# Performance work log

Measured on AMD Instinct MI355X. Metric: run time of the kernel, lower is better.

Reference implementation:

```python
import jax, jax.numpy as jnp
import numpy as np

NUM_NODE = 100000
DEG = 16
E = NUM_NODE * DEG
IN_C = 128
HID_C = 128
NUM_REL = 8


def setup_inputs() -> dict:
    key = jax.random.key(0)
    k1, k2, k3, k4, k5, k6 = jax.random.split(key, 6)
    x = jax.random.normal(k1, (NUM_NODE, IN_C), dtype=jnp.float32)
    # glorot-style init for relation weights [num_rel, in, hid]
    scale = jnp.sqrt(6.0 / (IN_C + HID_C)).astype(jnp.float32)
    rel_weight = jax.random.uniform(k2, (NUM_REL, IN_C, HID_C), dtype=jnp.float32, minval=-1.0, maxval=1.0) * scale
    # uniform-degree CSR so every node has deg >= 1 (avoids div-by-zero, matches module assumption)
    ptr = jnp.arange(NUM_NODE + 1, dtype=jnp.int64) * DEG
    idx = jax.random.randint(k3, (E,), 0, NUM_NODE, dtype=jnp.int64)
    edge_types = jax.random.randint(k4, (E,), 0, NUM_REL, dtype=jnp.int64)
    # about 1/3 of nodes have cached history (value != -1)
    history_map = jax.random.randint(k5, (NUM_NODE,), -1, 2, dtype=jnp.int64)
    history_buffer = jax.random.normal(k6, (NUM_NODE, HID_C), dtype=jnp.float32)
    return {
        'x': x,
        'rel_weight': rel_weight,
        'ptr': ptr,
        'idx': idx,
        'edge_types': edge_types,
        'history_map': history_map,
        'history_buffer': history_buffer,
        'history_size': 1,
        'num_node': NUM_NODE,
    }


def reference(x, rel_weight, ptr, idx, edge_types, history_map, history_buffer, history_size, num_node):
    E_ = idx.shape[0]
    num_rel = rel_weight.shape[0]
    hid = rel_weight.shape[2]
    xg = x[idx]                                   # [E, in] gather of source features
    # relation-grouped transform: small static loop over relations, masked accumulate
    msgs = jnp.zeros((E_, hid), dtype=x.dtype)
    for r in range(num_rel):
        msgs = msgs + jnp.where((edge_types == r)[:, None], xg @ rel_weight[r], jnp.zeros((), x.dtype))
    deg = ptr[1:] - ptr[:-1]                      # [num_node]
    seg = jnp.repeat(jnp.arange(num_node), deg, total_repeat_length=E_)  # dst id per edge
    out = jax.ops.segment_sum(msgs, seg, num_segments=num_node)          # scatter-sum
    out = out / deg[:, None].astype(out.dtype)    # degree normalization
    if history_size > 0:                          # static python int
        out = jnp.where((history_map != -1)[:, None], history_buffer, out)
    return (out, out)
```

## Files before the change

### kernel.cpp

```cpp
#include <hip/hip_runtime.h>
#include <stdint.h>

#define IN_C   128
#define HID_C  128
#define NREL   8
#define K_TOTAL (NREL * IN_C)
#define KHALF   512
#define TILE_M  16
#define SROW    520

typedef float  f32x4  __attribute__((ext_vector_type(4)));
typedef __bf16 bf16x8 __attribute__((ext_vector_type(8)));
typedef short  s16x8  __attribute__((ext_vector_type(8)));

__device__ __forceinline__ unsigned short f2bf(float f) {
    unsigned int u = __float_as_uint(f);
    u += 0x7fffu + ((u >> 16) & 1u);
    return (unsigned short)(u >> 16);
}

__global__ void zero_count_kernel(unsigned int* count) { *count = 0u; }

__global__ __launch_bounds__(256) void prep_kernel(
        const float* __restrict__ W, const int* __restrict__ hmap,
        unsigned short* __restrict__ Wt, int* __restrict__ list,
        unsigned int* __restrict__ count, int NN, int WE) {
    int tid = blockIdx.x * blockDim.x + threadIdx.x;
    if (tid < NN) {
        if (hmap[tid] == -1) {
            unsigned int p = atomicAdd(count, 1u);
            list[p] = tid;
        }
    }
    if (tid < WE) {
        int r   = tid >> 14;
        int rem = tid & 16383;
        int k   = rem >> 7;
        int c   = rem & 127;
        Wt[(size_t)c * K_TOTAL + r * IN_C + k] = f2bf(W[tid]);
    }
}

__global__ __launch_bounds__(256) void history_kernel(
        const int* __restrict__ hmap, const float* __restrict__ hbuf,
        float* __restrict__ out, int NN) {
    int gid = blockIdx.x * blockDim.x + threadIdx.x;
    int n = gid >> 5;
    int q = gid & 31;
    if (n >= NN) return;
    if (hmap[n] != -1) {
        const f32x4* src = (const f32x4*)hbuf;
        f32x4 v = src[(size_t)n * 32 + q];
        f32x4* o = (f32x4*)out;
        o[(size_t)n * 32 + q] = v;
        o[(size_t)NN * 32 + (size_t)n * 32 + q] = v;
    }
}

__global__ __launch_bounds__(256) void gemm_kernel(
        const float* __restrict__ x,
        const int* __restrict__ ptr,
        const int* __restrict__ idx,
        const int* __restrict__ ety,
        const unsigned short* __restrict__ Wt,
        const int* __restrict__ list,
        const unsigned int* __restrict__ count,
        float* __restrict__ out, int NN) {
    __shared__ float S[TILE_M * SROW];
    __shared__ int   nids[TILE_M];
    __shared__ float invdeg[TILE_M];

    unsigned int cnt = *count;
    int rowbase = blockIdx.x * TILE_M;
    if (rowbase >= (int)cnt) return;

    int t = threadIdx.x;
    if (t < TILE_M) {
        int row = rowbase + t;
        int nid = -1; float idg = 0.f;
        if (row < (int)cnt) {
            nid = list[row];
            int d = ptr[nid + 1] - ptr[nid];
            idg = 1.0f / (float)d;
        }
        nids[t] = nid;
        invdeg[t] = idg;
    }

    f32x4 acc0 = {0.f, 0.f, 0.f, 0.f};
    f32x4 acc1 = {0.f, 0.f, 0.f, 0.f};
    int wave   = t >> 6;
    int lane   = t & 63;
    int chbase = wave * 32;
    int quad   = lane >> 4;
    int l16    = lane & 15;

    int gn = t >> 4;
    int gc = (t & 15) * 8;

    for (int pass = 0; pass < 2; ++pass) {
        __syncthreads();
        for (int i = t; i < TILE_M * SROW / 4; i += 256)
            ((f32x4*)S)[i] = f32x4{0.f, 0.f, 0.f, 0.f};
        __syncthreads();
        int nid = nids[gn];
        if (nid >= 0) {
            int e0 = ptr[nid];
            int e1 = ptr[nid + 1];
            for (int e = e0; e < e1; ++e) {
                int r = ety[e];
                if ((r >> 2) != pass) continue;
                int src = idx[e];
                const float* xp = x + (size_t)src * IN_C + gc;
                float* sp = S + gn * SROW + (r & 3) * IN_C + gc;
                f32x4 a0 = *(const f32x4*)(xp);
                f32x4 a1 = *(const f32x4*)(xp + 4);
                *(f32x4*)(sp)     += a0;
                *(f32x4*)(sp + 4) += a1;
            }
        }
        __syncthreads();
        const float* arow = S + l16 * SROW + quad * 8;
        const unsigned short* bbase =
            Wt + (size_t)(chbase + l16) * K_TOTAL + pass * KHALF + quad * 8;
        for (int ks = 0; ks < KHALF; ks += 32) {
            const float* ap = arow + ks;
            f32x4 lo = *(const f32x4*)ap;
            f32x4 hi = *(const f32x4*)(ap + 4);
            s16x8 a;
            a[0] = (short)f2bf(lo[0]); a[1] = (short)f2bf(lo[1]);
            a[2] = (short)f2bf(lo[2]); a[3] = (short)f2bf(lo[3]);
            a[4] = (short)f2bf(hi[0]); a[5] = (short)f2bf(hi[1]);
            a[6] = (short)f2bf(hi[2]); a[7] = (short)f2bf(hi[3]);
            s16x8 b0 = *(const s16x8*)(bbase + ks);
            s16x8 b1 = *(const s16x8*)(bbase + ks + 16 * K_TOTAL);
            union { s16x8 s; bf16x8 b; } ua, ub0, ub1;
            ua.s = a; ub0.s = b0; ub1.s = b1;
            acc0 = __builtin_amdgcn_mfma_f32_16x16x32_bf16(ua.b, ub0.b, acc0, 0, 0, 0);
            acc1 = __builtin_amdgcn_mfma_f32_16x16x32_bf16(ua.b, ub1.b, acc1, 0, 0, 0);
        }
    }

    size_t half = (size_t)NN * HID_C;
    #pragma unroll
    for (int v = 0; v < 4; ++v) {
        int rowl = quad * 4 + v;
        int nid = nids[rowl];
        if (nid < 0) continue;
        float s = invdeg[rowl];
        float v0 = acc0[v] * s;
        float v1 = acc1[v] * s;
        size_t o0 = (size_t)nid * HID_C + chbase + l16;
        out[o0]           = v0;
        out[o0 + 16]      = v1;
        out[o0 + half]        = v0;
        out[o0 + 16 + half]   = v1;
    }
}

extern "C" void kernel_launch(void* const* d_in, const int* in_sizes, int n_in,
                              void* d_out, int out_size, void* d_ws, size_t ws_size,
                              hipStream_t stream) {
    const float* x    = (const float*)d_in[0];
    const float* W    = (const float*)d_in[1];
    const int*   ptr  = (const int*)d_in[2];
    const int*   idx  = (const int*)d_in[3];
    const int*   ety  = (const int*)d_in[4];
    const int*   hmap = (const int*)d_in[5];
    const float* hbuf = (const float*)d_in[6];
    int NN = in_sizes[5];
    int WE = in_sizes[1];
    float* out = (float*)d_out;

    unsigned int* count = (unsigned int*)d_ws;
    int* list = (int*)((char*)d_ws + 256);
    size_t wt_off = 256 + (((size_t)NN * 4 + 4095) / 4096) * 4096;
    unsigned short* Wt = (unsigned short*)((char*)d_ws + wt_off);

    zero_count_kernel<<<1, 1, 0, stream>>>(count);

    int total = WE > NN ? WE : NN;
    prep_kernel<<<(total + 255) / 256, 256, 0, stream>>>(W, hmap, Wt, list, count, NN, WE);
    history_kernel<<<((size_t)NN * 32 + 255) / 256, 256, 0, stream>>>(hmap, hbuf, out, NN);
    gemm_kernel<<<(NN + TILE_M - 1) / TILE_M, 256, 0, stream>>>(
        x, ptr, idx, ety, Wt, list, count, out, NN);
}
```

Baseline: 363.0 us.

## Accumulate per-relation sums in registers, single bf16 LDS pass, wave-aggregated atomics

The gather phase now accumulates neighbour features for all 8 relations in per-thread registers, masked by relation. It replaces the two-pass fp32 shared-memory read-modify-write scheme and its zeroing. Edge metadata (source id and relation packed into one word) is staged cooperatively in shared memory so edge loads are spread across threads. The sums are converted to bf16 once into a half-size LDS tile, and a single MFMA loop covers the full K=1024. The compaction of non-history nodes uses one wave-level ballot and atomic instead of one atomic per thread. The register arrays (64 floats per thread) raise register pressure and may reduce occupancy, and the masked FMAs across all relations add ALU work.

```diff
diff --git a/kernel.cpp b/kernel.cpp
--- a/kernel.cpp
+++ b/kernel.cpp
@@ -5,13 +5,13 @@
 #define HID_C  128
 #define NREL   8
 #define K_TOTAL (NREL * IN_C)
-#define KHALF   512
 #define TILE_M  16
-#define SROW    520
+#define SRB     1032
 
 typedef float  f32x4  __attribute__((ext_vector_type(4)));
 typedef __bf16 bf16x8 __attribute__((ext_vector_type(8)));
 typedef short  s16x8  __attribute__((ext_vector_type(8)));
+typedef unsigned short u16;
 
 __device__ __forceinline__ unsigned short f2bf(float f) {
     unsigned int u = __float_as_uint(f);
@@ -26,12 +26,21 @@
         unsigned short* __restrict__ Wt, int* __restrict__ list,
         unsigned int* __restrict__ count, int NN, int WE) {
     int tid = blockIdx.x * blockDim.x + threadIdx.x;
-    if (tid < NN) {
-        if (hmap[tid] == -1) {
-            unsigned int p = atomicAdd(count, 1u);
-            list[p] = tid;
-        }
-    }
+
+    bool active = (tid < NN) && (hmap[tid] == -1);
+    unsigned long long mask = __ballot(active);
+    if (mask) {
+        int lane   = threadIdx.x & 63;
+        int leader = __ffsll((unsigned long long)mask) - 1;
+        unsigned base = 0;
+        if (lane == leader) base = atomicAdd(count, (unsigned)__popcll(mask));
+        base = __shfl(base, leader, 64);
+        if (active) {
+            int off = __popcll(mask & ((1ull << lane) - 1ull));
+            list[base + off] = tid;
+        }
+    }
+
     if (tid < WE) {
         int r   = tid >> 14;
         int rem = tid & 16383;
@@ -66,9 +75,11 @@
         const int* __restrict__ list,
         const unsigned int* __restrict__ count,
         float* __restrict__ out, int NN) {
-    __shared__ float S[TILE_M * SROW];
-    __shared__ int   nids[TILE_M];
-    __shared__ float invdeg[TILE_M];
+    __shared__ u16      S[TILE_M * SRB];
+    __shared__ unsigned meta[TILE_M * 16];
+    __shared__ int      nids[TILE_M];
+    __shared__ int      degs[TILE_M];
+    __shared__ float    invdeg[TILE_M];
 
     unsigned int cnt = *count;
     int rowbase = blockIdx.x * TILE_M;
@@ -77,84 +88,108 @@
     int t = threadIdx.x;
     if (t < TILE_M) {
         int row = rowbase + t;
-        int nid = -1; float idg = 0.f;
+        int nid = -1, d = 0; float idg = 0.f;
         if (row < (int)cnt) {
             nid = list[row];
-            int d = ptr[nid + 1] - ptr[nid];
-            idg = 1.0f / (float)d;
-        }
-        nids[t] = nid;
-        invdeg[t] = idg;
-    }
-
-    f32x4 acc0 = {0.f, 0.f, 0.f, 0.f};
-    f32x4 acc1 = {0.f, 0.f, 0.f, 0.f};
-    int wave   = t >> 6;
-    int lane   = t & 63;
+            int e0 = ptr[nid], e1 = ptr[nid + 1];
+            d = e1 - e0;
+            idg = (d > 0) ? 1.0f / (float)d : 0.f;
+        }
+        nids[t] = nid; degs[t] = d; invdeg[t] = idg;
+    }
+    __syncthreads();
+
+    int n = t >> 4;
+    int c = t & 15;
+    int nid = nids[n];
+    int deg = degs[n];
+    int e0  = (nid >= 0) ? ptr[nid] : 0;
+
+    int maxdeg = 0;
+    #pragma unroll
+    for (int i = 0; i < TILE_M; ++i) maxdeg = max(maxdeg, degs[i]);
+
+    f32x4 alo[NREL], ahi[NREL];
+    #pragma unroll
+    for (int r = 0; r < NREL; ++r) { alo[r] = f32x4{0,0,0,0}; ahi[r] = f32x4{0,0,0,0}; }
+
+    for (int jb = 0; jb < maxdeg; jb += 16) {
+        {
+            int j = jb + c;
+            unsigned m = 0xFFFFFFFFu;
+            if (nid >= 0 && j < deg) {
+                int e = e0 + j;
+                m = ((unsigned)idx[e]) | (((unsigned)ety[e]) << 27);
+            }
+            meta[t] = m;
+        }
+        __syncthreads();
+        #pragma unroll 4
+        for (int j = 0; j < 16; ++j) {
+            unsigned m = meta[(n << 4) + j];
+            if (m == 0xFFFFFFFFu) continue;
+            int src = (int)(m & 0x07FFFFFFu);
+            int r   = (int)(m >> 27);
+            const f32x4* xp = (const f32x4*)(x + (size_t)src * IN_C + c * 8);
+            f32x4 a0 = xp[0];
+            f32x4 a1 = xp[1];
+            #pragma unroll
+            for (int rr = 0; rr < NREL; ++rr) {
+                float mk = (r == rr) ? 1.0f : 0.0f;
+                alo[rr] += a0 * mk;
+                ahi[rr] += a1 * mk;
+            }
+        }
+        __syncthreads();
+    }
+
+    {
+        u16* srow = S + n * SRB + c * 8;
+        #pragma unroll
+        for (int rr = 0; rr < NREL; ++rr) {
+            s16x8 pk;
+            pk[0] = (short)f2bf(alo[rr][0]); pk[1] = (short)f2bf(alo[rr][1]);
+            pk[2] = (short)f2bf(alo[rr][2]); pk[3] = (short)f2bf(alo[rr][3]);
+            pk[4] = (short)f2bf(ahi[rr][0]); pk[5] = (short)f2bf(ahi[rr][1]);
+            pk[6] = (short)f2bf(ahi[rr][2]); pk[7] = (short)f2bf(ahi[rr][3]);
+            *(s16x8*)(srow + rr * IN_C) = pk;
+        }
+    }
+    __syncthreads();
+
+    int wave = t >> 6, lane = t & 63;
+    int quad = lane >> 4, l16 = lane & 15;
     int chbase = wave * 32;
-    int quad   = lane >> 4;
-    int l16    = lane & 15;
-
-    int gn = t >> 4;
-    int gc = (t & 15) * 8;
-
-    for (int pass = 0; pass < 2; ++pass) {
-        __syncthreads();
-        for (int i = t; i < TILE_M * SROW / 4; i += 256)
-            ((f32x4*)S)[i] = f32x4{0.f, 0.f, 0.f, 0.f};
-        __syncthreads();
-        int nid = nids[gn];
-        if (nid >= 0) {
-            int e0 = ptr[nid];
-            int e1 = ptr[nid + 1];
-            for (int e = e0; e < e1; ++e) {
-                int r = ety[e];
-                if ((r >> 2) != pass) continue;
-                int src = idx[e];
-                const float* xp = x + (size_t)src * IN_C + gc;
-                float* sp = S + gn * SROW + (r & 3) * IN_C + gc;
-                f32x4 a0 = *(const f32x4*)(xp);
-                f32x4 a1 = *(const f32x4*)(xp + 4);
-                *(f32x4*)(sp)     += a0;
-                *(f32x4*)(sp + 4) += a1;
-            }
-        }
-        __syncthreads();
-        const float* arow = S + l16 * SROW + quad * 8;
-        const unsigned short* bbase =
-            Wt + (size_t)(chbase + l16) * K_TOTAL + pass * KHALF + quad * 8;
-        for (int ks = 0; ks < KHALF; ks += 32) {
-            const float* ap = arow + ks;
-            f32x4 lo = *(const f32x4*)ap;
-            f32x4 hi = *(const f32x4*)(ap + 4);
-            s16x8 a;
-            a[0] = (short)f2bf(lo[0]); a[1] = (short)f2bf(lo[1]);
-            a[2] = (short)f2bf(lo[2]); a[3] = (short)f2bf(lo[3]);
-            a[4] = (short)f2bf(hi[0]); a[5] = (short)f2bf(hi[1]);
-            a[6] = (short)f2bf(hi[2]); a[7] = (short)f2bf(hi[3]);
-            s16x8 b0 = *(const s16x8*)(bbase + ks);
-            s16x8 b1 = *(const s16x8*)(bbase + ks + 16 * K_TOTAL);
-            union { s16x8 s; bf16x8 b; } ua, ub0, ub1;
-            ua.s = a; ub0.s = b0; ub1.s = b1;
-            acc0 = __builtin_amdgcn_mfma_f32_16x16x32_bf16(ua.b, ub0.b, acc0, 0, 0, 0);
-            acc1 = __builtin_amdgcn_mfma_f32_16x16x32_bf16(ua.b, ub1.b, acc1, 0, 0, 0);
-        }
+    const u16* arow  = S + l16 * SRB + quad * 8;
+    const u16* bbase = Wt + (size_t)(chbase + l16) * K_TOTAL + quad * 8;
+
+    f32x4 acc0 = {0.f,0.f,0.f,0.f};
+    f32x4 acc1 = {0.f,0.f,0.f,0.f};
+    #pragma unroll 4
+    for (int ks = 0; ks < K_TOTAL; ks += 32) {
+        s16x8 a  = *(const s16x8*)(arow + ks);
+        s16x8 b0 = *(const s16x8*)(bbase + ks);
+        s16x8 b1 = *(const s16x8*)(bbase + ks + 16 * K_TOTAL);
+        union { s16x8 s; bf16x8 b; } ua, ub0, ub1;
+        ua.s = a; ub0.s = b0; ub1.s = b1;
+        acc0 = __builtin_amdgcn_mfma_f32_16x16x32_bf16(ua.b, ub0.b, acc0, 0, 0, 0);
+        acc1 = __builtin_amdgcn_mfma_f32_16x16x32_bf16(ua.b, ub1.b, acc1, 0, 0, 0);
     }
 
     size_t half = (size_t)NN * HID_C;
     #pragma unroll
     for (int v = 0; v < 4; ++v) {
         int rowl = quad * 4 + v;
-        int nid = nids[rowl];
-        if (nid < 0) continue;
+        int onid = nids[rowl];
+        if (onid < 0) continue;
         float s = invdeg[rowl];
         float v0 = acc0[v] * s;
         float v1 = acc1[v] * s;
-        size_t o0 = (size_t)nid * HID_C + chbase + l16;
-        out[o0]           = v0;
-        out[o0 + 16]      = v1;
-        out[o0 + half]        = v0;
-        out[o0 + 16 + half]   = v1;
+        size_t o0 = (size_t)onid * HID_C + chbase + l16;
+        out[o0]             = v0;
+        out[o0 + 16]        = v1;
+        out[o0 + half]      = v0;
+        out[o0 + 16 + half] = v1;
     }
 }
 
```

New measurement: 310.0 us. 14.6% less time.
